# Optimization experiments

Measured on AMD Instinct MI355X. Metric: run time of the kernel, lower is better.

## Reference

```python
import jax, jax.numpy as jnp
import numpy as np

N, D, H, E = 4096, 256, 8, 131072
HD = D // H
EPS = 1e-5


def layernorm(x, g, b):
    mu = jnp.mean(x, axis=-1, keepdims=True)
    var = jnp.mean((x - mu) ** 2, axis=-1, keepdims=True)
    return (x - mu) * jax.lax.rsqrt(var + EPS) * g + b


def setup_inputs() -> dict:
    key = jax.random.key(0)
    ks = jax.random.split(key, 20)
    s = 1.0 / np.sqrt(D)
    x = jax.random.normal(ks[0], (N, D), jnp.float32)
    adj = jax.random.uniform(ks[1], (N, N)) < 0.01
    adj_mask = adj | jnp.eye(N, dtype=bool)  # self-loops keep softmax rows finite
    edge_index = jax.random.randint(ks[2], (2, E), 0, N, dtype=jnp.int64)
    edge_attr = jax.random.normal(ks[3], (E, D), jnp.float32)
    p = {
        'wq': jax.random.normal(ks[4], (D, D)) * s, 'bq': jnp.zeros((D,)),
        'wk': jax.random.normal(ks[5], (D, D)) * s, 'bk': jnp.zeros((D,)),
        'wv': jax.random.normal(ks[6], (D, D)) * s, 'bv': jnp.zeros((D,)),
        'wo': jax.random.normal(ks[7], (D, D)) * s, 'bo': jnp.zeros((D,)),
        'we': jax.random.normal(ks[8], (D, H)) * s, 'be': jnp.zeros((H,)),
        'w1': jax.random.normal(ks[9], (D, 4 * D)) * s, 'b1': jnp.zeros((4 * D,)),
        'w2': jax.random.normal(ks[10], (4 * D, D)) * (1.0 / np.sqrt(4 * D)), 'b2': jnp.zeros((D,)),
        'g1': jnp.ones((D,)), 'beta1': jnp.zeros((D,)),
        'g2': jnp.ones((D,)), 'beta2': jnp.zeros((D,)),
    }
    return dict(x=x, adj_mask=adj_mask, edge_index=edge_index, edge_attr=edge_attr, **p)


def reference(x, adj_mask, edge_index, edge_attr, wq, bq, wk, bk, wv, bv, wo, bo,
              we, be, w1, b1, w2, b2, g1, beta1, g2, beta2):
    n = x.shape[0]
    Q = (x @ wq + bq).reshape(n, H, HD)
    K = (x @ wk + bk).reshape(n, H, HD)
    V = (x @ wv + bv).reshape(n, H, HD)
    scores = jnp.einsum('nhd,mhd->nmh', Q, K) / np.sqrt(HD)  # [N,N,H]
    edge_bias = edge_attr @ we + be                          # [E,H]
    scores = scores.at[edge_index[0], edge_index[1]].add(edge_bias)
    s = jnp.transpose(scores, (0, 2, 1))                     # [N,H,N]
    s = jnp.where(adj_mask[:, None, :], s, -jnp.inf)
    attn = jax.nn.softmax(s, axis=-1)                        # dropout eval-mode no-op
    ctx = jnp.einsum('nhm,mhd->nhd', attn, V).reshape(n, D)
    attn_out = ctx @ wo + bo
    x1 = layernorm(x + attn_out, g1, beta1)
    ff = jax.nn.gelu(x1 @ w1 + b1, approximate=False) @ w2 + b2
    return layernorm(x1 + ff, g2, beta2)
```

## Files before the change

kernel.cpp:

```cpp
#include <hip/hip_runtime.h>
#include <math.h>

#define NN   4096
#define DD   256
#define HH   8
#define HD   32
#define DFF  1024
#define QKVW 768
#define AC   128
#define EC   128
#define SCPAD 129
#define QSP  36
#define NPB  2

typedef unsigned short ushort_t;
typedef __attribute__((ext_vector_type(8))) short short8;
typedef __attribute__((ext_vector_type(4))) float f32x4;

__device__ __forceinline__ float bf2f(unsigned short u){
  union { unsigned int i; float f; } v; v.i = ((unsigned int)u) << 16; return v.f;
}
__device__ __forceinline__ unsigned short f2bf(float f){
  union { float f; unsigned int i; } v; v.f = f;
  unsigned int x = v.i;
  return (unsigned short)((x + 0x7FFFu + ((x >> 16) & 1u)) >> 16);
}
__device__ __forceinline__ float ldf(const void* p, size_t i, int isbf){
  return isbf ? bf2f(((const ushort_t*)p)[i]) : ((const float*)p)[i];
}
__device__ __forceinline__ ushort_t ldb16(const void* p, size_t i, int isbf){
  return isbf ? ((const ushort_t*)p)[i] : f2bf(((const float*)p)[i]);
}

__global__ void k_detect(const int* __restrict__ adj32, const int* __restrict__ ei32,
                         const unsigned int* __restrict__ g1w, int* __restrict__ flags,
                         int* __restrict__ counts, int* __restrict__ cursor){
  __shared__ int c0s, c1s;
  int t = threadIdx.x;
  if (t == 0) { c0s = 0; c1s = 0; }
  __syncthreads();
  int c0 = 0, c1 = 0;
  for (int i = t; i < 960; i += 256) if (adj32[(size_t)i * 4097] != 0) c0++;
  for (int i = t; i < 2048; i += 256) if (ei32[2*i + 1] != 0) c1++;
  atomicAdd(&c0s, c0); atomicAdd(&c1s, c1);
  for (int i = t; i < NN; i += 256) { counts[i] = 0; cursor[i] = 0; }
  __syncthreads();
  if (t == 0) {
    flags[0] = (c0s == 960) ? 1 : 0;
    flags[1] = (c1s > 100) ? 1 : 0;
    flags[2] = (g1w[0] == 0x3F803F80u) ? 1 : 0;
  }
}

__global__ __launch_bounds__(256) void k_csr(const void* __restrict__ adj,
                                             const int* __restrict__ flags,
                                             int* __restrict__ alist,
                                             int* __restrict__ acnt){
  __shared__ int cntS;
  __shared__ int actS[AC];
  const int n = blockIdx.x, t = threadIdx.x;
  if (t == 0) cntS = 0;
  __syncthreads();
  if (flags[0]) {
    const uint4* arow = (const uint4*)((const int*)adj + (size_t)n * NN);
    #pragma unroll
    for (int i = 0; i < 4; i++) {
      uint4 v = arow[t + 256 * i];
      int c0 = 4 * (t + 256 * i);
      if (v.x) { int p = atomicAdd(&cntS, 1); if (p < AC) actS[p] = c0; }
      if (v.y) { int p = atomicAdd(&cntS, 1); if (p < AC) actS[p] = c0 + 1; }
      if (v.z) { int p = atomicAdd(&cntS, 1); if (p < AC) actS[p] = c0 + 2; }
      if (v.w) { int p = atomicAdd(&cntS, 1); if (p < AC) actS[p] = c0 + 3; }
    }
  } else {
    const uint4* arow = (const uint4*)((const unsigned char*)adj + (size_t)n * NN);
    uint4 v = arow[t];
    unsigned int wsv[4] = {v.x, v.y, v.z, v.w};
    #pragma unroll
    for (int q = 0; q < 4; q++) {
      unsigned int u = wsv[q];
      int c0 = 16 * t + 4 * q;
      if (u & 0x000000FFu) { int p = atomicAdd(&cntS, 1); if (p < AC) actS[p] = c0; }
      if (u & 0x0000FF00u) { int p = atomicAdd(&cntS, 1); if (p < AC) actS[p] = c0 + 1; }
      if (u & 0x00FF0000u) { int p = atomicAdd(&cntS, 1); if (p < AC) actS[p] = c0 + 2; }
      if (u & 0xFF000000u) { int p = atomicAdd(&cntS, 1); if (p < AC) actS[p] = c0 + 3; }
    }
  }
  __syncthreads();
  int m = cntS; if (m > AC) m = AC;
  if (t == 0) acnt[n] = m;
  for (int j = t; j < m; j += 256) alist[(size_t)n * AC + j] = actS[j];
}

#define NX    (NN * DD)
#define NWE   (DD * HH)
#define TPREP 768
__global__ __launch_bounds__(256) void k_prep(
    const void* __restrict__ x, const void* __restrict__ wq, const void* __restrict__ wk,
    const void* __restrict__ wv, const void* __restrict__ wo, const void* __restrict__ w1,
    const void* __restrict__ w2, const void* __restrict__ we,
    const void* __restrict__ bq, const void* __restrict__ bk, const void* __restrict__ bv,
    const void* __restrict__ bo, const void* __restrict__ be, const void* __restrict__ b1,
    const void* __restrict__ b2, const void* __restrict__ g1, const void* __restrict__ be1,
    const void* __restrict__ g2, const void* __restrict__ be2,
    const int* __restrict__ ei, const int* __restrict__ flags,
    ushort_t* __restrict__ xb,
    ushort_t* __restrict__ wqkvT, ushort_t* __restrict__ woT,
    ushort_t* __restrict__ w1T, ushort_t* __restrict__ w2T,
    float* __restrict__ wef, float* __restrict__ bqkvf,
    float* __restrict__ bof, float* __restrict__ bef,
    float* __restrict__ b1f, float* __restrict__ b2f,
    float* __restrict__ g1f, float* __restrict__ be1f,
    float* __restrict__ g2f, float* __restrict__ be2f,
    int* __restrict__ counts, int E, int TOT)
{
  const int isbf = flags[2];
  const int t = threadIdx.x;
  if (blockIdx.x < TPREP) {
    __shared__ ushort_t tile[32][36];
    int b = blockIdx.x;
    const void* src; ushort_t* dst; int R, C, ti;
    if (b < 64)       { src = wq; dst = wqkvT;              R = 256;  C = 256;  ti = b; }
    else if (b < 128) { src = wk; dst = wqkvT + 256 * 256;  R = 256;  C = 256;  ti = b - 64; }
    else if (b < 192) { src = wv; dst = wqkvT + 512 * 256;  R = 256;  C = 256;  ti = b - 128; }
    else if (b < 256) { src = wo; dst = woT;                R = 256;  C = 256;  ti = b - 192; }
    else if (b < 512) { src = w1; dst = w1T;                R = 256;  C = 1024; ti = b - 256; }
    else              { src = w2; dst = w2T;                R = 1024; C = 256;  ti = b - 512; }
    int tiles_c = C >> 5;
    int tr = ti / tiles_c, tc = ti - tr * tiles_c;
    int lr = t >> 3, lc0 = (t & 7) << 2;
    size_t sbase = (size_t)(tr * 32 + lr) * C + tc * 32 + lc0;
    if (isbf) {
      const ushort_t* s16 = (const ushort_t*)src + sbase;
      tile[lr][lc0+0] = s16[0]; tile[lr][lc0+1] = s16[1];
      tile[lr][lc0+2] = s16[2]; tile[lr][lc0+3] = s16[3];
    } else {
      const float4* sf = (const float4*)((const float*)src + sbase);
      float4 v = *sf;
      tile[lr][lc0+0] = f2bf(v.x); tile[lr][lc0+1] = f2bf(v.y);
      tile[lr][lc0+2] = f2bf(v.z); tile[lr][lc0+3] = f2bf(v.w);
    }
    __syncthreads();
    int i = t >> 3, j0 = (t & 7) << 2;
    ushort_t* dp = dst + (size_t)(tc * 32 + i) * R + tr * 32 + j0;
    ushort_t o0 = tile[j0][i], o1 = tile[j0+1][i], o2 = tile[j0+2][i], o3 = tile[j0+3][i];
    dp[0] = o0; dp[1] = o1; dp[2] = o2; dp[3] = o3;
    return;
  }
  const int ei32 = flags[1];
  const int stride = (gridDim.x - TPREP) * 256;
  for (int i = (blockIdx.x - TPREP) * 256 + t; i < TOT; i += stride) {
    int r = i;
    if (r < NX) { xb[r] = ldb16(x, r, isbf); continue; }
    r -= NX;
    if (r < E) {
      int src = ei32 ? ei[r] : ei[2 * r];
      if ((unsigned)src < (unsigned)NN) atomicAdd(&counts[src], 1);
      continue;
    }
    r -= E;
    if (r < NWE) { wef[r] = ldf(we, r, isbf); continue; }
    r -= NWE;
    if (r < QKVW) {
      const void* bs = (r < 256) ? bq : (r < 512) ? bk : bv;
      bqkvf[r] = ldf(bs, r & 255, isbf);
      continue;
    }
    r -= QKVW;
    if (r < DD)  { bof[r] = ldf(bo, r, isbf); continue; }   r -= DD;
    if (r < HH)  { bef[r] = ldf(be, r, isbf); continue; }   r -= HH;
    if (r < DFF) { b1f[r] = ldf(b1, r, isbf); continue; }   r -= DFF;
    if (r < DD)  { b2f[r] = ldf(b2, r, isbf); continue; }   r -= DD;
    if (r < DD)  { g1f[r] = ldf(g1, r, isbf); continue; }   r -= DD;
    if (r < DD)  { be1f[r] = ldf(be1, r, isbf); continue; } r -= DD;
    if (r < DD)  { g2f[r] = ldf(g2, r, isbf); continue; }   r -= DD;
    if (r < DD)  { be2f[r] = ldf(be2, r, isbf); }
  }
}

#define LDT 40
__global__ __launch_bounds__(256) void k_gemm64(
    const ushort_t* __restrict__ A, const ushort_t* __restrict__ Bt,
    const float* __restrict__ bias, void* __restrict__ C,
    int M, int Nn, int K, int act, int mode,
    float* __restrict__ qf, ushort_t* __restrict__ kbuf, ushort_t* __restrict__ vbuf)
{
  __shared__ ushort_t As[64 * LDT];
  __shared__ ushort_t Bs[64 * LDT];
  const int t = threadIdx.x;
  const int wave = t >> 6, lane = t & 63;
  const int wr = wave >> 1, wc = wave & 1;
  const int l15 = lane & 15, quad = lane >> 4;
  const int bm0 = blockIdx.y * 64, bn0 = blockIdx.x * 64;
  const int row = t >> 2, kg = (t & 3) << 3;

  f32x4 acc[2][2] = {};

  const ushort_t* ap = A  + (size_t)(bm0 + row) * K + kg;
  const ushort_t* bp = Bt + (size_t)(bn0 + row) * K + kg;
  uint4 av = *(const uint4*)ap;
  uint4 bv = *(const uint4*)bp;

  for (int k0 = 0; k0 < K; k0 += 32) {
    __syncthreads();
    *(uint4*)(&As[row * LDT + kg]) = av;
    *(uint4*)(&Bs[row * LDT + kg]) = bv;
    __syncthreads();
    if (k0 + 32 < K) {
      av = *(const uint4*)(ap + k0 + 32);
      bv = *(const uint4*)(bp + k0 + 32);
    }
    short8 af0 = *(const short8*)(&As[(wr * 32 +      l15) * LDT + quad * 8]);
    short8 af1 = *(const short8*)(&As[(wr * 32 + 16 + l15) * LDT + quad * 8]);
    short8 bf0 = *(const short8*)(&Bs[(wc * 32 +      l15) * LDT + quad * 8]);
    short8 bf1 = *(const short8*)(&Bs[(wc * 32 + 16 + l15) * LDT + quad * 8]);
    acc[0][0] = __builtin_amdgcn_mfma_f32_16x16x32_bf16(af0, bf0, acc[0][0], 0, 0, 0);
    acc[0][1] = __builtin_amdgcn_mfma_f32_16x16x32_bf16(af0, bf1, acc[0][1], 0, 0, 0);
    acc[1][0] = __builtin_amdgcn_mfma_f32_16x16x32_bf16(af1, bf0, acc[1][0], 0, 0, 0);
    acc[1][1] = __builtin_amdgcn_mfma_f32_16x16x32_bf16(af1, bf1, acc[1][1], 0, 0, 0);
  }

  #pragma unroll
  for (int fr = 0; fr < 2; fr++) {
    #pragma unroll
    for (int fc = 0; fc < 2; fc++) {
      int gn = bn0 + wc * 32 + fc * 16 + l15;
      float bcol = bias[gn];
      #pragma unroll
      for (int r = 0; r < 4; r++) {
        int gm = bm0 + wr * 32 + fr * 16 + quad * 4 + r;
        float v = acc[fr][fc][r] + bcol;
        if (act) v = 0.5f * v * (1.0f + erff(v * 0.70710678118654752f));
        if (mode == 2) {
          if (gn < 256)      qf[(size_t)gm * 256 + gn] = v;
          else if (gn < 512) kbuf[(size_t)gm * 256 + (gn - 256)] = f2bf(v);
          else               vbuf[(size_t)gm * 256 + (gn - 512)] = f2bf(v);
        } else if (mode == 1) {
          ((ushort_t*)C)[(size_t)gm * Nn + gn] = f2bf(v);
        } else {
          ((float*)C)[(size_t)gm * Nn + gn] = v;
        }
      }
    }
  }
}

__global__ __launch_bounds__(256) void k_scan(const int* __restrict__ counts,
                                              int* __restrict__ off){
  __shared__ int part[256];
  int t = threadIdx.x;
  int loc[16]; int s = 0;
  #pragma unroll
  for (int j = 0; j < 16; j++) { loc[j] = counts[t * 16 + j]; s += loc[j]; }
  part[t] = s;
  __syncthreads();
  if (t == 0) {
    int run = 0;
    for (int i = 0; i < 256; i++) { int tmp = part[i]; part[i] = run; run += tmp; }
  }
  __syncthreads();
  int base = part[t];
  if (t == 0) off[0] = 0;
  #pragma unroll
  for (int j = 0; j < 16; j++) { base += loc[j]; off[t * 16 + j + 1] = base; }
}

__global__ void k_scatter(const int* __restrict__ ei, const int* __restrict__ flags,
                          const int* __restrict__ off, int* __restrict__ cursor,
                          int* __restrict__ sdst, int* __restrict__ seid, int e){
  int i = blockIdx.x * 256 + threadIdx.x;
  if (i >= e) return;
  int src, dst;
  if (flags[1]) { src = ei[i];     dst = ei[e + i]; }
  else          { src = ei[2 * i]; dst = ei[2 * (e + i)]; }
  if ((unsigned)src >= (unsigned)NN) return;
  if ((unsigned)dst >= (unsigned)NN) dst = 0;
  int pos = off[src] + atomicAdd(&cursor[src], 1);
  sdst[pos] = dst; seid[pos] = i;
}

__global__ __launch_bounds__(256) void k_ebias(
    const void* __restrict__ ea, const float* __restrict__ wef,
    const float* __restrict__ bef, float* __restrict__ sbias,
    int E, const int* __restrict__ flags)
{
  __shared__ float wel[HH * DD];
  int t = threadIdx.x;
  #pragma unroll
  for (int j = 0; j < 8; j++) wel[j * DD + t] = wef[t * 8 + j];
  const int isbf = flags[2];
  __syncthreads();
  int idx = blockIdx.x * 256 + t;
  int e = idx >> 3, p = idx & 7;
  float acc[8] = {};
  if (e < E) {
    if (isbf) {
      const uint4* base = (const uint4*)((const ushort_t*)ea + (size_t)e * DD);
      #pragma unroll
      for (int q = 0; q < 4; q++) {
        uint4 u = base[q * 8 + p];
        int dbase = 64 * q + 8 * p;
        float f[8];
        union { unsigned int i; float f; } cv;
        cv.i = u.x << 16; f[0] = cv.f; cv.i = u.x & 0xFFFF0000u; f[1] = cv.f;
        cv.i = u.y << 16; f[2] = cv.f; cv.i = u.y & 0xFFFF0000u; f[3] = cv.f;
        cv.i = u.z << 16; f[4] = cv.f; cv.i = u.z & 0xFFFF0000u; f[5] = cv.f;
        cv.i = u.w << 16; f[6] = cv.f; cv.i = u.w & 0xFFFF0000u; f[7] = cv.f;
        #pragma unroll
        for (int j = 0; j < 8; j++)
          #pragma unroll
          for (int h = 0; h < 8; h++)
            acc[h] = fmaf(f[j], wel[h * DD + dbase + j], acc[h]);
      }
    } else {
      const float4* base = (const float4*)((const float*)ea + (size_t)e * DD);
      #pragma unroll
      for (int q = 0; q < 8; q++) {
        float4 u = base[q * 8 + p];
        int dbase = 32 * q + 4 * p;
        #pragma unroll
        for (int h = 0; h < 8; h++) {
          acc[h] = fmaf(u.x, wel[h * DD + dbase + 0], acc[h]);
          acc[h] = fmaf(u.y, wel[h * DD + dbase + 1], acc[h]);
          acc[h] = fmaf(u.z, wel[h * DD + dbase + 2], acc[h]);
          acc[h] = fmaf(u.w, wel[h * DD + dbase + 3], acc[h]);
        }
      }
    }
  }
  #pragma unroll
  for (int h = 0; h < 8; h++) {
    acc[h] += __shfl_xor(acc[h], 1, 8);
    acc[h] += __shfl_xor(acc[h], 2, 8);
    acc[h] += __shfl_xor(acc[h], 4, 8);
  }
  if (e < E) sbias[(size_t)e * 8 + p] = acc[p] + bef[p];
}

__global__ __launch_bounds__(256) void k_attn(
    const float* __restrict__ qf, const ushort_t* __restrict__ kb,
    const ushort_t* __restrict__ vb,
    const int* __restrict__ alist, const int* __restrict__ acnt,
    const int* __restrict__ off, const int* __restrict__ sdst,
    const int* __restrict__ seid, const float* __restrict__ sbias,
    ushort_t* __restrict__ ctxb)
{
  __shared__ float qs[NPB][HH * QSP];
  __shared__ int   act[NPB][AC];
  __shared__ float sc[NPB][HH][SCPAD];
  __shared__ int   edst[NPB][EC];
  __shared__ float ivs[NPB][HH];

  const int t = threadIdx.x;
  const int n0 = blockIdx.x * NPB;

  int na[NPB], cn[NPB], st[NPB];
  #pragma unroll
  for (int s = 0; s < NPB; s++) {
    int n = n0 + s;
    qs[s][(t >> 5) * QSP + (t & 31)] = qf[(size_t)n * DD + t];
    na[s] = min(acnt[n], AC);
    st[s] = off[n];
    int c = off[n + 1] - st[s];
    cn[s] = c < 0 ? 0 : (c > EC ? EC : c);
    for (int j = t; j < na[s]; j += 256) act[s][j] = alist[(size_t)n * AC + j];
    for (int j = t; j < cn[s]; j += 256) edst[s][j] = sdst[st[s] + j];
  }
  __syncthreads();

  #pragma unroll
  for (int s = 0; s < NPB; s++) {
    for (int item = t; item < na[s] * HH; item += 256) {
      int idx = item >> 3, h = item & 7;
      int m = act[s][idx];
      const uint4* kr = (const uint4*)(kb + (size_t)m * DD + h * HD);
      const float* qh = qs[s] + h * QSP;
      float a = 0.f;
      #pragma unroll
      for (int q4 = 0; q4 < 4; q4++) {
        uint4 u = kr[q4];
        int b = q4 * 8;
        union { unsigned int i; float f; } cv;
        cv.i = u.x << 16;         a = fmaf(cv.f, qh[b+0], a);
        cv.i = u.x & 0xFFFF0000u; a = fmaf(cv.f, qh[b+1], a);
        cv.i = u.y << 16;         a = fmaf(cv.f, qh[b+2], a);
        cv.i = u.y & 0xFFFF0000u; a = fmaf(cv.f, qh[b+3], a);
        cv.i = u.z << 16;         a = fmaf(cv.f, qh[b+4], a);
        cv.i = u.z & 0xFFFF0000u; a = fmaf(cv.f, qh[b+5], a);
        cv.i = u.w << 16;         a = fmaf(cv.f, qh[b+6], a);
        cv.i = u.w & 0xFFFF0000u; a = fmaf(cv.f, qh[b+7], a);
      }
      sc[s][h][idx] = a * 0.17677669529663687f;
    }
  }
  __syncthreads();

  #pragma unroll
  for (int s = 0; s < NPB; s++) {
    for (int item = t; item < cn[s] * HH; item += 256) {
      int j = item >> 3, h = item & 7;
      int sid = seid[st[s] + j];
      int dst = edst[s][j];
      int pos = -1;
      for (int i = 0; i < na[s]; i++) if (act[s][i] == dst) { pos = i; break; }
      if (pos >= 0) atomicAdd(&sc[s][h][pos], sbias[(size_t)sid * 8 + h]);
    }
  }
  __syncthreads();

  #pragma unroll
  for (int s = 0; s < NPB; s++) {
    const int h = t >> 5, l = t & 31;
    float lm = -1e30f;
    for (int i = l; i < na[s]; i += 32) lm = fmaxf(lm, sc[s][h][i]);
    #pragma unroll
    for (int o = 16; o > 0; o >>= 1) lm = fmaxf(lm, __shfl_down(lm, o, 32));
    lm = __shfl(lm, 0, 32);
    float ls = 0.f;
    for (int i = l; i < na[s]; i += 32) {
      float e = __expf(sc[s][h][i] - lm);
      sc[s][h][i] = e;
      ls += e;
    }
    #pragma unroll
    for (int o = 16; o > 0; o >>= 1) ls += __shfl_down(ls, o, 32);
    if (l == 0) ivs[s][h] = 1.0f / ls;
  }
  __syncthreads();

  #pragma unroll
  for (int s = 0; s < NPB; s++) {
    const int h = t >> 5, d = t & 31;
    const ushort_t* vcol = vb + h * HD + d;
    const float* scp = sc[s][h];
    float acc = 0.f;
    int i = 0;
    for (; i + 8 <= na[s]; i += 8) {
      int mm[8]; float vv[8];
      #pragma unroll
      for (int u = 0; u < 8; u++) mm[u] = act[s][i + u];
      #pragma unroll
      for (int u = 0; u < 8; u++) vv[u] = bf2f(vcol[(size_t)mm[u] * DD]);
      #pragma unroll
      for (int u = 0; u < 8; u++) acc = fmaf(scp[i + u], vv[u], acc);
    }
    for (; i < na[s]; i++)
      acc = fmaf(scp[i], bf2f(vcol[(size_t)act[s][i] * DD]), acc);
    ctxb[(size_t)(n0 + s) * DD + h * HD + d] = f2bf(acc * ivs[s][h]);
  }
}

__global__ __launch_bounds__(256) void k_ln(
    const void* __restrict__ a, const float* __restrict__ b,
    const float* __restrict__ g, const float* __restrict__ beta,
    void* __restrict__ out, ushort_t* __restrict__ out_b,
    int a_raw, int final_mode, const int* __restrict__ flags)
{
  __shared__ float rw[4];
  __shared__ float mu_s, var_s;
  const int n = blockIdx.x, t = threadIdx.x;
  const int wid = t >> 6, lid = t & 63;
  float av = a_raw ? ldf(a, (size_t)n * DD + t, flags[2])
                   : ((const float*)a)[(size_t)n * DD + t];
  float v = av + b[(size_t)n * DD + t];
  float s = v;
  #pragma unroll
  for (int o = 32; o > 0; o >>= 1) s += __shfl_down(s, o, 64);
  if (lid == 0) rw[wid] = s;
  __syncthreads();
  if (t == 0) mu_s = (rw[0] + rw[1] + rw[2] + rw[3]) * (1.0f / 256.0f);
  __syncthreads();
  const float mu = mu_s;
  const float dv = v - mu;
  float q = dv * dv;
  #pragma unroll
  for (int o = 32; o > 0; o >>= 1) q += __shfl_down(q, o, 64);
  if (lid == 0) rw[wid] = q;
  __syncthreads();
  if (t == 0) var_s = (rw[0] + rw[1] + rw[2] + rw[3]) * (1.0f / 256.0f);
  __syncthreads();
  float res = dv * rsqrtf(var_s + 1e-5f) * g[t] + beta[t];
  if (final_mode && flags[2])
    ((ushort_t*)out)[(size_t)n * DD + t] = f2bf(res);
  else
    ((float*)out)[(size_t)n * DD + t] = res;
  if (out_b) out_b[(size_t)n * DD + t] = f2bf(res);
}

extern "C" void kernel_launch(void* const* d_in, const int* in_sizes, int n_in,
                              void* d_out, int out_size, void* d_ws, size_t ws_size,
                              hipStream_t stream)
{
  const void* x   = d_in[0];
  const void* adj = d_in[1];
  const int*  ei  = (const int*)d_in[2];
  const void* ea  = d_in[3];
  const void* wq  = d_in[4];  const void* bq  = d_in[5];
  const void* wk  = d_in[6];  const void* bk  = d_in[7];
  const void* wv  = d_in[8];  const void* bv  = d_in[9];
  const void* wo  = d_in[10]; const void* bo  = d_in[11];
  const void* we  = d_in[12]; const void* be  = d_in[13];
  const void* w1  = d_in[14]; const void* b1  = d_in[15];
  const void* w2  = d_in[16]; const void* b2  = d_in[17];
  const void* g1  = d_in[18]; const void* be1 = d_in[19];
  const void* g2  = d_in[20]; const void* be2 = d_in[21];
  const int E = in_sizes[2] / 2;

  char* w = (char*)d_ws;
  size_t o = 0;
  auto carve = [&](size_t bytes) -> void* {
    void* p = w + o; o = (o + bytes + 255) & ~(size_t)255; return p;
  };
  ushort_t* xb    = (ushort_t*)carve((size_t)NN * DD * 2);
  float*    qfb   = (float*)   carve((size_t)NN * DD * 4);
  ushort_t* kbuf  = (ushort_t*)carve((size_t)NN * DD * 2);
  ushort_t* vbuf  = (ushort_t*)carve((size_t)NN * DD * 2);
  ushort_t* wqkvT = (ushort_t*)carve((size_t)QKVW * DD * 2);
  float*    bqkvf = (float*)   carve(QKVW * 4);
  ushort_t* woT   = (ushort_t*)carve((size_t)DD * DD * 2);
  ushort_t* w1T   = (ushort_t*)carve((size_t)DFF * DD * 2);
  ushort_t* w2T   = (ushort_t*)carve((size_t)DD * DFF * 2);
  float*    wef   = (float*)   carve((size_t)DD * HH * 4);
  float*    bof   = (float*)   carve(DD * 4);
  float*    bef   = (float*)   carve(HH * 4);
  float*    b1f   = (float*)   carve(DFF * 4);
  float*    b2f   = (float*)   carve(DD * 4);
  float*    g1f   = (float*)   carve(DD * 4);
  float*    be1f  = (float*)   carve(DD * 4);
  float*    g2f   = (float*)   carve(DD * 4);
  float*    be2f  = (float*)   carve(DD * 4);
  int*      counts = (int*)carve((size_t)NN * 4);
  int*      cursor = (int*)carve((size_t)NN * 4);
  int*      off    = (int*)carve((size_t)(NN + 1) * 4);
  int*      sdst   = (int*)carve((size_t)E * 4);
  int*      seid   = (int*)carve((size_t)E * 4);
  float*    sbias  = (float*)carve((size_t)E * HH * 4);
  int*      alist  = (int*)carve((size_t)NN * AC * 4);
  int*      acnt   = (int*)carve((size_t)NN * 4);
  ushort_t* ctxb     = (ushort_t*)carve((size_t)NN * DD * 2);
  float*    attn_out = (float*)   carve((size_t)NN * DD * 4);
  float*    x1f      = (float*)   carve((size_t)NN * DD * 4);
  ushort_t* x1b      = (ushort_t*)carve((size_t)NN * DD * 2);
  ushort_t* hbufb    = (ushort_t*)carve((size_t)NN * DFF * 2);
  float*    ff2o     = (float*)   carve((size_t)NN * DD * 4);
  int*      flags    = (int*)carve(4 * 4);

  k_detect<<<1, 256, 0, stream>>>((const int*)adj, ei, (const unsigned int*)g1,
                                  flags, counts, cursor);
  k_csr<<<NN, 256, 0, stream>>>(adj, flags, alist, acnt);

  const int TOT = NX + E + NWE + QKVW + DD + HH + DFF + DD + DD + DD + DD + DD;
  k_prep<<<TPREP + 1280, 256, 0, stream>>>(
      x, wq, wk, wv, wo, w1, w2, we, bq, bk, bv, bo, be, b1, b2,
      g1, be1, g2, be2, ei, flags,
      xb, wqkvT, woT, w1T, w2T, wef, bqkvf,
      bof, bef, b1f, b2f, g1f, be1f, g2f, be2f, counts, E, TOT);

  k_scan<<<1, 256, 0, stream>>>(counts, off);
  int eb = (E + 255) / 256;
  k_scatter<<<eb, 256, 0, stream>>>(ei, flags, off, cursor, sdst, seid, E);
  k_ebias<<<(E * 8 + 255) / 256, 256, 0, stream>>>(ea, wef, bef, sbias, E, flags);

  k_gemm64<<<dim3(QKVW / 64, NN / 64), 256, 0, stream>>>(
      xb, wqkvT, bqkvf, nullptr, NN, QKVW, DD, 0, 2, qfb, kbuf, vbuf);

  k_attn<<<NN / NPB, 256, 0, stream>>>(qfb, kbuf, vbuf, alist, acnt, off, sdst,
                                       seid, sbias, ctxb);

  k_gemm64<<<dim3(DD / 64, NN / 64), 256, 0, stream>>>(
      ctxb, woT, bof, attn_out, NN, DD, DD, 0, 0, nullptr, nullptr, nullptr);
  k_ln<<<NN, 256, 0, stream>>>(x, attn_out, g1f, be1f, x1f, x1b, 1, 0, flags);
  k_gemm64<<<dim3(DFF / 64, NN / 64), 256, 0, stream>>>(
      x1b, w1T, b1f, hbufb, NN, DFF, DD, 1, 1, nullptr, nullptr, nullptr);
  k_gemm64<<<dim3(DD / 64, NN / 64), 256, 0, stream>>>(
      hbufb, w2T, b2f, ff2o, NN, DD, DFF, 0, 0, nullptr, nullptr, nullptr);
  k_ln<<<NN, 256, 0, stream>>>(x1f, ff2o, g2f, be2f, d_out, (ushort_t*)nullptr, 0, 1, flags);
}
```

Baseline: 437.6 us.

## Deepen GEMM K-step, add 32-row tile variant, vectorize attention V gather, warp-scan offsets

The GEMM kernel becomes a template that stages 64-wide K slices per sync, halving barrier count, and adds a BM=32 variant used for the narrow N=256 outputs so more blocks are launched. The attention context loop now has each thread handle two adjacent head dims with 32-bit V loads and covers both nodes of the block at once. The single-thread serial prefix in k_scan is replaced with wave shuffles. These target barrier overhead, low occupancy on narrow GEMMs, and scalar gather traffic, at the cost of more LDS per block and somewhat more registers.

```diff
diff --git a/kernel.cpp b/kernel.cpp
--- a/kernel.cpp
+++ b/kernel.cpp
@@ -178,53 +178,74 @@
   }
 }
 
-#define LDT 40
-__global__ __launch_bounds__(256) void k_gemm64(
+#define LDK 72
+template<int BM>
+__global__ __launch_bounds__(256) void k_gemm(
     const ushort_t* __restrict__ A, const ushort_t* __restrict__ Bt,
     const float* __restrict__ bias, void* __restrict__ C,
     int M, int Nn, int K, int act, int mode,
     float* __restrict__ qf, ushort_t* __restrict__ kbuf, ushort_t* __restrict__ vbuf)
 {
-  __shared__ ushort_t As[64 * LDT];
-  __shared__ ushort_t Bs[64 * LDT];
+  constexpr int NF = (BM == 64) ? 2 : 1;
+  constexpr int CW = (BM == 64) ? 32 : 16;
+  __shared__ ushort_t As[BM * LDK];
+  __shared__ ushort_t Bs[64 * LDK];
   const int t = threadIdx.x;
   const int wave = t >> 6, lane = t & 63;
-  const int wr = wave >> 1, wc = wave & 1;
   const int l15 = lane & 15, quad = lane >> 4;
-  const int bm0 = blockIdx.y * 64, bn0 = blockIdx.x * 64;
-  const int row = t >> 2, kg = (t & 3) << 3;
-
-  f32x4 acc[2][2] = {};
-
-  const ushort_t* ap = A  + (size_t)(bm0 + row) * K + kg;
-  const ushort_t* bp = Bt + (size_t)(bn0 + row) * K + kg;
-  uint4 av = *(const uint4*)ap;
-  uint4 bv = *(const uint4*)bp;
-
-  for (int k0 = 0; k0 < K; k0 += 32) {
+  const int wr = (BM == 64) ? (wave >> 1) : 0;
+  const int wc = (BM == 64) ? (wave & 1) : wave;
+  const int bm0 = blockIdx.y * BM, bn0 = blockIdx.x * 64;
+
+  const int arow = (BM == 64) ? (t >> 2) : (t >> 3);
+  const int akg  = (BM == 64) ? ((t & 3) << 4) : ((t & 7) << 3);
+  const int brow = t >> 2, bkg = (t & 3) << 4;
+
+  f32x4 acc[2][NF] = {};
+
+  const ushort_t* ap = A  + (size_t)(bm0 + arow) * K + akg;
+  const ushort_t* bp = Bt + (size_t)(bn0 + brow) * K + bkg;
+  uint4 a0 = *(const uint4*)ap;
+  uint4 a1{};
+  if constexpr (BM == 64) a1 = *(const uint4*)(ap + 8);
+  uint4 b0 = *(const uint4*)bp;
+  uint4 b1 = *(const uint4*)(bp + 8);
+
+  for (int k0 = 0; k0 < K; k0 += 64) {
     __syncthreads();
-    *(uint4*)(&As[row * LDT + kg]) = av;
-    *(uint4*)(&Bs[row * LDT + kg]) = bv;
+    *(uint4*)(&As[arow * LDK + akg]) = a0;
+    if constexpr (BM == 64) *(uint4*)(&As[arow * LDK + akg + 8]) = a1;
+    *(uint4*)(&Bs[brow * LDK + bkg]) = b0;
+    *(uint4*)(&Bs[brow * LDK + bkg + 8]) = b1;
     __syncthreads();
-    if (k0 + 32 < K) {
-      av = *(const uint4*)(ap + k0 + 32);
-      bv = *(const uint4*)(bp + k0 + 32);
-    }
-    short8 af0 = *(const short8*)(&As[(wr * 32 +      l15) * LDT + quad * 8]);
-    short8 af1 = *(const short8*)(&As[(wr * 32 + 16 + l15) * LDT + quad * 8]);
-    short8 bf0 = *(const short8*)(&Bs[(wc * 32 +      l15) * LDT + quad * 8]);
-    short8 bf1 = *(const short8*)(&Bs[(wc * 32 + 16 + l15) * LDT + quad * 8]);
-    acc[0][0] = __builtin_amdgcn_mfma_f32_16x16x32_bf16(af0, bf0, acc[0][0], 0, 0, 0);
-    acc[0][1] = __builtin_amdgcn_mfma_f32_16x16x32_bf16(af0, bf1, acc[0][1], 0, 0, 0);
-    acc[1][0] = __builtin_amdgcn_mfma_f32_16x16x32_bf16(af1, bf0, acc[1][0], 0, 0, 0);
-    acc[1][1] = __builtin_amdgcn_mfma_f32_16x16x32_bf16(af1, bf1, acc[1][1], 0, 0, 0);
+    if (k0 + 64 < K) {
+      a0 = *(const uint4*)(ap + k0 + 64);
+      if constexpr (BM == 64) a1 = *(const uint4*)(ap + k0 + 64 + 8);
+      b0 = *(const uint4*)(bp + k0 + 64);
+      b1 = *(const uint4*)(bp + k0 + 64 + 8);
+    }
+    #pragma unroll
+    for (int kk = 0; kk < 2; kk++) {
+      short8 af[2], bf[NF];
+      #pragma unroll
+      for (int fr = 0; fr < 2; fr++)
+        af[fr] = *(const short8*)(&As[(wr * 32 + fr * 16 + l15) * LDK + kk * 32 + quad * 8]);
+      #pragma unroll
+      for (int fc = 0; fc < NF; fc++)
+        bf[fc] = *(const short8*)(&Bs[(wc * CW + fc * 16 + l15) * LDK + kk * 32 + quad * 8]);
+      #pragma unroll
+      for (int fr = 0; fr < 2; fr++)
+        #pragma unroll
+        for (int fc = 0; fc < NF; fc++)
+          acc[fr][fc] = __builtin_amdgcn_mfma_f32_16x16x32_bf16(af[fr], bf[fc], acc[fr][fc], 0, 0, 0);
+    }
   }
 
   #pragma unroll
   for (int fr = 0; fr < 2; fr++) {
     #pragma unroll
-    for (int fc = 0; fc < 2; fc++) {
-      int gn = bn0 + wc * 32 + fc * 16 + l15;
+    for (int fc = 0; fc < NF; fc++) {
+      int gn = bn0 + wc * CW + fc * 16 + l15;
       float bcol = bias[gn];
       #pragma unroll
       for (int r = 0; r < 4; r++) {
@@ -247,22 +268,26 @@
 
 __global__ __launch_bounds__(256) void k_scan(const int* __restrict__ counts,
                                               int* __restrict__ off){
-  __shared__ int part[256];
-  int t = threadIdx.x;
+  __shared__ int wsum[4];
+  const int t = threadIdx.x, lid = t & 63, wid = t >> 6;
   int loc[16]; int s = 0;
   #pragma unroll
   for (int j = 0; j < 16; j++) { loc[j] = counts[t * 16 + j]; s += loc[j]; }
-  part[t] = s;
-  __syncthreads();
-  if (t == 0) {
-    int run = 0;
-    for (int i = 0; i < 256; i++) { int tmp = part[i]; part[i] = run; run += tmp; }
-  }
-  __syncthreads();
-  int base = part[t];
+  const int tot = s;
+  #pragma unroll
+  for (int o = 1; o < 64; o <<= 1) {
+    int u = __shfl_up(s, o, 64);
+    if (lid >= o) s += u;
+  }
+  if (lid == 63) wsum[wid] = s;
+  __syncthreads();
+  int pre = 0;
+  #pragma unroll
+  for (int w = 0; w < 4; w++) if (w < wid) pre += wsum[w];
+  int run = pre + s - tot;
   if (t == 0) off[0] = 0;
   #pragma unroll
-  for (int j = 0; j < 16; j++) { base += loc[j]; off[t * 16 + j + 1] = base; }
+  for (int j = 0; j < 16; j++) { run += loc[j]; off[t * 16 + j + 1] = run; }
 }
 
 __global__ void k_scatter(const int* __restrict__ ei, const int* __restrict__ flags,
@@ -428,25 +453,35 @@
   }
   __syncthreads();
 
-  #pragma unroll
-  for (int s = 0; s < NPB; s++) {
-    const int h = t >> 5, d = t & 31;
-    const ushort_t* vcol = vb + h * HD + d;
-    const float* scp = sc[s][h];
-    float acc = 0.f;
+  {
+    const int s_ = t >> 7, h = (t >> 4) & 7, dp = t & 15;
+    const int n_a = s_ ? na[1] : na[0];
+    const ushort_t* vcol = vb + h * HD + 2 * dp;
+    const float* scp = sc[s_][h];
+    float a0 = 0.f, a1 = 0.f;
     int i = 0;
-    for (; i + 8 <= na[s]; i += 8) {
-      int mm[8]; float vv[8];
-      #pragma unroll
-      for (int u = 0; u < 8; u++) mm[u] = act[s][i + u];
-      #pragma unroll
-      for (int u = 0; u < 8; u++) vv[u] = bf2f(vcol[(size_t)mm[u] * DD]);
-      #pragma unroll
-      for (int u = 0; u < 8; u++) acc = fmaf(scp[i + u], vv[u], acc);
-    }
-    for (; i < na[s]; i++)
-      acc = fmaf(scp[i], bf2f(vcol[(size_t)act[s][i] * DD]), acc);
-    ctxb[(size_t)(n0 + s) * DD + h * HD + d] = f2bf(acc * ivs[s][h]);
+    for (; i + 8 <= n_a; i += 8) {
+      int mm[8]; unsigned int vv[8];
+      #pragma unroll
+      for (int u = 0; u < 8; u++) mm[u] = act[s_][i + u];
+      #pragma unroll
+      for (int u = 0; u < 8; u++) vv[u] = *(const unsigned int*)(vcol + (size_t)mm[u] * DD);
+      #pragma unroll
+      for (int u = 0; u < 8; u++) {
+        float p = scp[i + u];
+        a0 = fmaf(p, bf2f((ushort_t)(vv[u] & 0xFFFFu)), a0);
+        a1 = fmaf(p, bf2f((ushort_t)(vv[u] >> 16)), a1);
+      }
+    }
+    for (; i < n_a; i++) {
+      unsigned int v = *(const unsigned int*)(vcol + (size_t)act[s_][i] * DD);
+      float p = scp[i];
+      a0 = fmaf(p, bf2f((ushort_t)(v & 0xFFFFu)), a0);
+      a1 = fmaf(p, bf2f((ushort_t)(v >> 16)), a1);
+    }
+    float iv = ivs[s_][h];
+    unsigned int ob = ((unsigned int)f2bf(a1 * iv) << 16) | (unsigned int)f2bf(a0 * iv);
+    *(unsigned int*)(ctxb + (size_t)(n0 + s_) * DD + h * HD + 2 * dp) = ob;
   }
 }
 
@@ -561,18 +596,18 @@
   k_scatter<<<eb, 256, 0, stream>>>(ei, flags, off, cursor, sdst, seid, E);
   k_ebias<<<(E * 8 + 255) / 256, 256, 0, stream>>>(ea, wef, bef, sbias, E, flags);
 
-  k_gemm64<<<dim3(QKVW / 64, NN / 64), 256, 0, stream>>>(
+  k_gemm<64><<<dim3(QKVW / 64, NN / 64), 256, 0, stream>>>(
       xb, wqkvT, bqkvf, nullptr, NN, QKVW, DD, 0, 2, qfb, kbuf, vbuf);
 
   k_attn<<<NN / NPB, 256, 0, stream>>>(qfb, kbuf, vbuf, alist, acnt, off, sdst,
                                        seid, sbias, ctxb);
 
-  k_gemm64<<<dim3(DD / 64, NN / 64), 256, 0, stream>>>(
+  k_gemm<32><<<dim3(DD / 64, NN / 32), 256, 0, stream>>>(
       ctxb, woT, bof, attn_out, NN, DD, DD, 0, 0, nullptr, nullptr, nullptr);
   k_ln<<<NN, 256, 0, stream>>>(x, attn_out, g1f, be1f, x1f, x1b, 1, 0, flags);
-  k_gemm64<<<dim3(DFF / 64, NN / 64), 256, 0, stream>>>(
+  k_gemm<64><<<dim3(DFF / 64, NN / 64), 256, 0, stream>>>(
       x1b, w1T, b1f, hbufb, NN, DFF, DD, 1, 1, nullptr, nullptr, nullptr);
-  k_gemm64<<<dim3(DD / 64, NN / 64), 256, 0, stream>>>(
+  k_gemm<32><<<dim3(DD / 64, NN / 32), 256, 0, stream>>>(
       hbufb, w2T, b2f, ff2o, NN, DD, DFF, 0, 0, nullptr, nullptr, nullptr);
   k_ln<<<NN, 256, 0, stream>>>(x1f, ff2o, g2f, be2f, d_out, (ushort_t*)nullptr, 0, 1, flags);
 }
```

After: 419.3 us. 1.04x faster.
